# Optimization experiments

Measured on AMD Instinct MI355X. Metric: run time of the kernel, lower is better.

The kernel has to match this reference:

```python
import jax, jax.numpy as jnp
import numpy as np

B, SQ, SK, D = 8, 4096, 4096, 64


def setup_inputs() -> dict:
    key = jax.random.key(0)
    k1, k2, k3 = jax.random.split(key, 3)
    x1 = jax.random.normal(k1, (B, SQ, D), dtype=jnp.float32)   # queries
    x2 = jax.random.normal(k2, (B, SK, D), dtype=jnp.float32)   # keys
    x3 = jax.random.normal(k3, (B, SK, D), dtype=jnp.float32)   # values
    x4 = 0                                                      # dropout p (static, 0 => deterministic)
    x5 = jnp.ones((1,), dtype=jnp.float32)                      # scale divisor
    return {"x1": x1, "x2": x2, "x3": x3, "x4": x4, "x5": x5}


def reference(x1, x2, x3, x4, x5):
    # scores: [B, Sq, Sk]
    scores = jnp.einsum("bqd,bkd->bqk", x1, x2) / x5
    attn = jax.nn.softmax(scores, axis=-1)
    p = float(x4)  # static python scalar
    if p > 0.0:
        mask = jax.random.bernoulli(jax.random.key(42), 1.0 - p, attn.shape)
        attn = attn * mask.astype(attn.dtype) / (1.0 - p)
    # out: [B, Sq, D]
    return jnp.einsum("bqk,bkd->bqd", attn, x3)
```

## Files before the change

### kernel.cpp

```cpp
#include <hip/hip_runtime.h>


typedef _Float16 f16x8 __attribute__((ext_vector_type(8)));
typedef _Float16 f16x4 __attribute__((ext_vector_type(4)));
typedef __fp16   h16x2 __attribute__((ext_vector_type(2)));
typedef float    f32x4 __attribute__((ext_vector_type(4)));

constexpr int kB  = 8;
constexpr int kSQ = 4096;
constexpr int kSK = 4096;
constexpr int kD  = 64;
constexpr int KSPLIT = 4;
constexpr int SKH = kSK / KSPLIT;
constexpr int BQ  = 128;
constexpr int BK  = 64;
constexpr size_t APART = (size_t)kB * kSQ * kD;
constexpr float kLog2e = 1.44269504088896340736f;

static __device__ __forceinline__ f16x4 pack4(float a, float b, float c, float d) {
    h16x2 p0 = __builtin_amdgcn_cvt_pkrtz(a, b);
    h16x2 p1 = __builtin_amdgcn_cvt_pkrtz(c, d);
    f16x4 r;
    r[0] = (_Float16)p0[0]; r[1] = (_Float16)p0[1];
    r[2] = (_Float16)p1[0]; r[3] = (_Float16)p1[1];
    return r;
}
static __device__ __forceinline__ f16x8 pack8(const float4& a, const float4& c) {
    f16x4 lo = pack4(a.x, a.y, a.z, a.w);
    f16x4 hi = pack4(c.x, c.y, c.z, c.w);
    f16x8 f;
    f[0] = lo[0]; f[1] = lo[1]; f[2] = lo[2]; f[3] = lo[3];
    f[4] = hi[0]; f[5] = hi[1]; f[6] = hi[2]; f[7] = hi[3];
    return f;
}

typedef const __attribute__((address_space(1))) unsigned int* gu32p;
typedef __attribute__((address_space(3))) unsigned int* lu32p;
static __device__ __forceinline__ void gload_lds16(const void* g, void* l) {
    __builtin_amdgcn_global_load_lds((gu32p)g, (lu32p)l, 16, 0, 0);
}

__global__ __launch_bounds__(256, 2)
void fattn_prepass(const float* __restrict__ Kg,
                   const float* __restrict__ Vg,
                   _Float16* __restrict__ Kh,
                   _Float16* __restrict__ Vt)
{
    __shared__ _Float16 tr[kD][BK];

    const int tid = threadIdx.x;
    const int kt  = blockIdx.x;
    const int b   = blockIdx.y;

    const int k = tid >> 2;
    const int p = tid & 3;
    const int gk = kt * BK + k;

    {
        const float* src = Kg + ((size_t)b * kSK + gk) * kD + p * 16;
        const float4 a0 = *(const float4*)(src + 0);
        const float4 a1 = *(const float4*)(src + 4);
        const float4 a2 = *(const float4*)(src + 8);
        const float4 a3 = *(const float4*)(src + 12);
        _Float16* dst = Kh + ((size_t)b * kSK + gk) * kD;
        const int fb0 = 2 * p, fb1 = 2 * p + 1;
        *(f16x8*)&dst[(fb0 ^ (gk & 7)) * 8] = pack8(a0, a1);
        *(f16x8*)&dst[(fb1 ^ (gk & 7)) * 8] = pack8(a2, a3);
    }
    {
        const float* src = Vg + ((size_t)b * kSK + gk) * kD + p * 16;
        const float4 a0 = *(const float4*)(src + 0);
        const float4 a1 = *(const float4*)(src + 4);
        const float4 a2 = *(const float4*)(src + 8);
        const float4 a3 = *(const float4*)(src + 12);
        const float v[16] = {a0.x,a0.y,a0.z,a0.w, a1.x,a1.y,a1.z,a1.w,
                             a2.x,a2.y,a2.z,a2.w, a3.x,a3.y,a3.z,a3.w};
#pragma unroll
        for (int j = 0; j < 16; ++j)
            tr[p * 16 + j][k] = (_Float16)v[j];
    }
    __syncthreads();
    {
        const int f  = tid >> 2;
        const int p2 = tid & 3;
        const f16x8 b0 = *(const f16x8*)&tr[f][p2 * 16 + 0];
        const f16x8 b1 = *(const f16x8*)&tr[f][p2 * 16 + 8];
        _Float16* dst = Vt + (((size_t)b * 64 + kt) * kD + f) * BK;
        const int kb0 = 2 * p2, kb1 = 2 * p2 + 1;
        *(f16x8*)&dst[(kb0 ^ (f & 7)) * 8] = b0;
        *(f16x8*)&dst[(kb1 ^ (f & 7)) * 8] = b1;
    }
}

__global__ __launch_bounds__(256, 4)
void fattn_partial(const float* __restrict__ Qg,
                   const _Float16* __restrict__ Kh,
                   const _Float16* __restrict__ Vt,
                   const float* __restrict__ sdiv,
                   _Float16* __restrict__ Ap,
                   float2* __restrict__ MLp)
{
    __shared__ __align__(16) _Float16 sK[2][BK * kD];
    __shared__ __align__(16) _Float16 sV[2][kD * BK];
    __shared__ __align__(16) _Float16 sP[4][16][BK];

    const int tid  = threadIdx.x;
    const int w    = tid >> 6;
    const int lane = tid & 63;
    const int l16  = lane & 15;
    const int quad = lane >> 4;
    const int sw   = (quad ^ (l16 & 7)) * 8;
    const int swp  = (l16 & 7) * 8;

    const int flat = blockIdx.x;
    const int c    = flat & 31;
    const int qi   = flat >> 5;
    const int b    = c >> 2;
    const int ks   = c & 3;
    const int qb   = qi * BQ;

    const float qscale = kLog2e / sdiv[0];

    const float* Qb = Qg + ((size_t)b * kSQ + qb) * kD;
    const _Float16* Khb = Kh + ((size_t)b * kSK + (size_t)ks * SKH) * kD;
    const _Float16* Vtb = Vt + (((size_t)b * 64 + (size_t)ks * (SKH / BK)) * kD) * BK;

    f16x8 qf[2][2];
#pragma unroll
    for (int mt = 0; mt < 2; ++mt) {
        const float* qrow = Qb + (size_t)(w * 32 + mt * 16 + l16) * kD;
#pragma unroll
        for (int kk = 0; kk < 2; ++kk) {
            const float4 a = *(const float4*)(qrow + kk * 32 + quad * 8);
            const float4 cc = *(const float4*)(qrow + kk * 32 + quad * 8 + 4);
            float4 as = make_float4(a.x * qscale, a.y * qscale, a.z * qscale, a.w * qscale);
            float4 cs = make_float4(cc.x * qscale, cc.y * qscale, cc.z * qscale, cc.w * qscale);
            qf[mt][kk] = pack8(as, cs);
        }
    }

    auto stage = [&](int kt, int buf) {
        const char* gk = (const char*)(Khb + (size_t)kt * BK * kD) + w * 2048 + lane * 16;
        const char* gv = (const char*)(Vtb + (size_t)kt * kD * BK) + w * 2048 + lane * 16;
        char* lk = (char*)&sK[buf][0] + w * 2048;
        char* lv = (char*)&sV[buf][0] + w * 2048;
        gload_lds16(gk,        lk);
        gload_lds16(gk + 1024, lk + 1024);
        gload_lds16(gv,        lv);
        gload_lds16(gv + 1024, lv + 1024);
    };

    f32x4 o[2][4];
    float m_i[2] = {-1e30f, -1e30f}, l_i[2] = {0.0f, 0.0f};
#pragma unroll
    for (int mt = 0; mt < 2; ++mt)
#pragma unroll
        for (int dt = 0; dt < 4; ++dt)
#pragma unroll
            for (int r = 0; r < 4; ++r) o[mt][dt][r] = 0.0f;

    stage(0, 0);
    __syncthreads();

    const int nIter = SKH / BK;
    for (int kt = 0; kt < nIter; ++kt) {
        const int buf = kt & 1;
        const bool more = (kt + 1 < nIter);
        if (more) stage(kt + 1, buf ^ 1);

        f32x4 s[2][4];
#pragma unroll
        for (int nt = 0; nt < 4; ++nt) {
            const int krow = (nt * 16 + l16) * kD;
            const f16x8 kf0 = *(const f16x8*)&sK[buf][krow + sw];
            const f16x8 kf1 = *(const f16x8*)&sK[buf][krow + (sw ^ 32)];
#pragma unroll
            for (int mt = 0; mt < 2; ++mt) {
                f32x4 acc;
#pragma unroll
                for (int r = 0; r < 4; ++r) acc[r] = 0.0f;
                acc = __builtin_amdgcn_mfma_f32_16x16x32_f16(kf0, qf[mt][0], acc, 0, 0, 0);
                acc = __builtin_amdgcn_mfma_f32_16x16x32_f16(kf1, qf[mt][1], acc, 0, 0, 0);
                s[mt][nt] = acc;
            }
        }

        f16x8 vf[4][2];
#pragma unroll
        for (int dt = 0; dt < 4; ++dt) {
            const int frow = (dt * 16 + l16) * BK;
            vf[dt][0] = *(const f16x8*)&sV[buf][frow + sw];
            vf[dt][1] = *(const f16x8*)&sV[buf][frow + (sw ^ 32)];
        }

#pragma unroll
        for (int mt = 0; mt < 2; ++mt) {
            float ra = fmaxf(fmaxf(s[mt][0][0], s[mt][0][1]), fmaxf(s[mt][0][2], s[mt][0][3]));
            float rb = fmaxf(fmaxf(s[mt][1][0], s[mt][1][1]), fmaxf(s[mt][1][2], s[mt][1][3]));
            float rc = fmaxf(fmaxf(s[mt][2][0], s[mt][2][1]), fmaxf(s[mt][2][2], s[mt][2][3]));
            float rd = fmaxf(fmaxf(s[mt][3][0], s[mt][3][1]), fmaxf(s[mt][3][2], s[mt][3][3]));
            float rm = fmaxf(fmaxf(ra, rb), fmaxf(rc, rd));
            rm = fmaxf(rm, __shfl_xor(rm, 16, 64));
            rm = fmaxf(rm, __shfl_xor(rm, 32, 64));
            const float mnew = fmaxf(m_i[mt], rm);
            float rs = 0.0f;
#pragma unroll
            for (int nt = 0; nt < 4; ++nt)
#pragma unroll
                for (int r = 0; r < 4; ++r) {
                    const float p = __builtin_amdgcn_exp2f(s[mt][nt][r] - mnew);
                    s[mt][nt][r] = p;
                    rs += p;
                }
            rs += __shfl_xor(rs, 16, 64);
            rs += __shfl_xor(rs, 32, 64);
            if (!__all(mnew == m_i[mt])) {
                const float alpha = __builtin_amdgcn_exp2f(m_i[mt] - mnew);
                l_i[mt] *= alpha;
#pragma unroll
                for (int dt = 0; dt < 4; ++dt)
#pragma unroll
                    for (int r = 0; r < 4; ++r) o[mt][dt][r] *= alpha;
            }
            m_i[mt] = mnew;
            l_i[mt] += rs;

#pragma unroll
            for (int nt = 0; nt < 4; ++nt)
                *(f16x4*)&sP[w][l16][(nt * 16 + quad * 4) ^ swp] =
                    pack4(s[mt][nt][0], s[mt][nt][1], s[mt][nt][2], s[mt][nt][3]);

            const f16x8 pf0 = *(const f16x8*)&sP[w][l16][(quad * 8) ^ swp];
            const f16x8 pf1 = *(const f16x8*)&sP[w][l16][(32 + quad * 8) ^ swp];
#pragma unroll
            for (int dt = 0; dt < 4; ++dt) {
                o[mt][dt] = __builtin_amdgcn_mfma_f32_16x16x32_f16(vf[dt][0], pf0, o[mt][dt], 0, 0, 0);
                o[mt][dt] = __builtin_amdgcn_mfma_f32_16x16x32_f16(vf[dt][1], pf1, o[mt][dt], 0, 0, 0);
            }
        }

        __syncthreads();
    }

    _Float16* Ab = Ap + (size_t)ks * APART + ((size_t)b * kSQ + qb) * kD;
    float2* MLb = MLp + (size_t)ks * kB * kSQ + (size_t)b * kSQ + qb;
#pragma unroll
    for (int mt = 0; mt < 2; ++mt) {
        const int row = w * 32 + mt * 16 + l16;
#pragma unroll
        for (int dt = 0; dt < 4; ++dt)
            *(f16x4*)&Ab[(size_t)row * kD + dt * 16 + quad * 4] =
                pack4(o[mt][dt][0], o[mt][dt][1], o[mt][dt][2], o[mt][dt][3]);
        if (quad == 0) MLb[row] = make_float2(m_i[mt], l_i[mt]);
    }
}

__global__ __launch_bounds__(256)
void fattn_combine(const _Float16* __restrict__ Ap,
                   const float2* __restrict__ MLp,
                   float* __restrict__ Og)
{
    const int idx = blockIdx.x * 256 + threadIdx.x;
    const int r = idx >> 4;
    const int c = (idx & 15) * 4;

    float m = -1e30f;
    float2 ml[KSPLIT];
#pragma unroll
    for (int s = 0; s < KSPLIT; ++s) {
        ml[s] = MLp[(size_t)s * kB * kSQ + r];
        m = fmaxf(m, ml[s].x);
    }
    float acc[4] = {0.f, 0.f, 0.f, 0.f};
    float lsum = 0.f;
#pragma unroll
    for (int s = 0; s < KSPLIT; ++s) {
        const float e = __builtin_amdgcn_exp2f(ml[s].x - m);
        lsum += e * ml[s].y;
        const f16x4 a = *(const f16x4*)&Ap[(size_t)s * APART + (size_t)r * kD + c];
#pragma unroll
        for (int j = 0; j < 4; ++j) acc[j] += e * (float)a[j];
    }
    const float inv = 1.0f / lsum;
    float4 res = make_float4(acc[0] * inv, acc[1] * inv, acc[2] * inv, acc[3] * inv);
    *(float4*)&Og[(size_t)r * kD + c] = res;
}

extern "C" void kernel_launch(void* const* d_in, const int* in_sizes, int n_in,
                              void* d_out, int out_size, void* d_ws, size_t ws_size,
                              hipStream_t stream) {
    const float* Q    = (const float*)d_in[0];
    const float* K    = (const float*)d_in[1];
    const float* V    = (const float*)d_in[2];
    const float* sdiv = (const float*)d_in[4];
    float* O = (float*)d_out;

    _Float16* Kh  = (_Float16*)d_ws;
    _Float16* Vt  = Kh + (size_t)kB * kSK * kD;
    _Float16* Ap  = Vt + (size_t)kB * kSK * kD;
    float2*   MLp = (float2*)(Ap + (size_t)KSPLIT * APART);

    fattn_prepass<<<dim3(kSK / BK, kB), dim3(256), 0, stream>>>(K, V, Kh, Vt);
    fattn_partial<<<dim3((kSQ / BQ) * kB * KSPLIT), dim3(256), 0, stream>>>(Q, Kh, Vt, sdiv, Ap, MLp);
    fattn_combine<<<dim3(kB * kSQ * kD / (256 * 4)), dim3(256), 0, stream>>>(Ap, MLp, O);
}
```

Before: 145.8 us.

## Double query tile per block and compute row sums with MFMA against ones

Each block now handles 256 query rows, so each wave holds four 16-row tiles instead of two. This doubles reuse of every K/V tile staged into LDS and halves global K/V traffic per query. The softmax row-sum no longer uses scalar adds and cross-lane shuffles; it runs as extra MFMAs that multiply P by a vector of ones into a separate accumulator. In exchange, register pressure rises (launch bounds drop from 4 to 2 blocks per SM), occupancy falls, there are half as many blocks, and the row sum is accumulated from fp16-rounded P.

```diff
diff --git a/kernel.cpp b/kernel.cpp
--- a/kernel.cpp
+++ b/kernel.cpp
@@ -12,7 +12,8 @@
 constexpr int kD  = 64;
 constexpr int KSPLIT = 4;
 constexpr int SKH = kSK / KSPLIT;
-constexpr int BQ  = 128;
+constexpr int BQ  = 256;
+constexpr int MT  = 4;
 constexpr int BK  = 64;
 constexpr size_t APART = (size_t)kB * kSQ * kD;
 constexpr float kLog2e = 1.44269504088896340736f;
@@ -92,7 +93,7 @@
     }
 }
 
-__global__ __launch_bounds__(256, 4)
+__global__ __launch_bounds__(256, 2)
 void fattn_partial(const float* __restrict__ Qg,
                    const _Float16* __restrict__ Kh,
                    const _Float16* __restrict__ Vt,
@@ -125,10 +126,10 @@
     const _Float16* Khb = Kh + ((size_t)b * kSK + (size_t)ks * SKH) * kD;
     const _Float16* Vtb = Vt + (((size_t)b * 64 + (size_t)ks * (SKH / BK)) * kD) * BK;
 
-    f16x8 qf[2][2];
-#pragma unroll
-    for (int mt = 0; mt < 2; ++mt) {
-        const float* qrow = Qb + (size_t)(w * 32 + mt * 16 + l16) * kD;
+    f16x8 qf[MT][2];
+#pragma unroll
+    for (int mt = 0; mt < MT; ++mt) {
+        const float* qrow = Qb + (size_t)(w * 64 + mt * 16 + l16) * kD;
 #pragma unroll
         for (int kk = 0; kk < 2; ++kk) {
             const float4 a = *(const float4*)(qrow + kk * 32 + quad * 8);
@@ -138,6 +139,10 @@
             qf[mt][kk] = pack8(as, cs);
         }
     }
+
+    f16x8 ones;
+#pragma unroll
+    for (int j = 0; j < 8; ++j) ones[j] = (_Float16)1.0f;
 
     auto stage = [&](int kt, int buf) {
         const char* gk = (const char*)(Khb + (size_t)kt * BK * kD) + w * 2048 + lane * 16;
@@ -150,14 +155,19 @@
         gload_lds16(gv + 1024, lv + 1024);
     };
 
-    f32x4 o[2][4];
-    float m_i[2] = {-1e30f, -1e30f}, l_i[2] = {0.0f, 0.0f};
-#pragma unroll
-    for (int mt = 0; mt < 2; ++mt)
+    f32x4 o[MT][4];
+    f32x4 ol[MT];
+    float m_i[MT];
+#pragma unroll
+    for (int mt = 0; mt < MT; ++mt) {
+        m_i[mt] = -1e30f;
+#pragma unroll
+        for (int r = 0; r < 4; ++r) ol[mt][r] = 0.0f;
 #pragma unroll
         for (int dt = 0; dt < 4; ++dt)
 #pragma unroll
             for (int r = 0; r < 4; ++r) o[mt][dt][r] = 0.0f;
+    }
 
     stage(0, 0);
     __syncthreads();
@@ -168,14 +178,14 @@
         const bool more = (kt + 1 < nIter);
         if (more) stage(kt + 1, buf ^ 1);
 
-        f32x4 s[2][4];
+        f32x4 s[MT][4];
 #pragma unroll
         for (int nt = 0; nt < 4; ++nt) {
             const int krow = (nt * 16 + l16) * kD;
             const f16x8 kf0 = *(const f16x8*)&sK[buf][krow + sw];
             const f16x8 kf1 = *(const f16x8*)&sK[buf][krow + (sw ^ 32)];
 #pragma unroll
-            for (int mt = 0; mt < 2; ++mt) {
+            for (int mt = 0; mt < MT; ++mt) {
                 f32x4 acc;
 #pragma unroll
                 for (int r = 0; r < 4; ++r) acc[r] = 0.0f;
@@ -194,7 +204,7 @@
         }
 
 #pragma unroll
-        for (int mt = 0; mt < 2; ++mt) {
+        for (int mt = 0; mt < MT; ++mt) {
             float ra = fmaxf(fmaxf(s[mt][0][0], s[mt][0][1]), fmaxf(s[mt][0][2], s[mt][0][3]));
             float rb = fmaxf(fmaxf(s[mt][1][0], s[mt][1][1]), fmaxf(s[mt][1][2], s[mt][1][3]));
             float rc = fmaxf(fmaxf(s[mt][2][0], s[mt][2][1]), fmaxf(s[mt][2][2], s[mt][2][3]));
@@ -203,27 +213,20 @@
             rm = fmaxf(rm, __shfl_xor(rm, 16, 64));
             rm = fmaxf(rm, __shfl_xor(rm, 32, 64));
             const float mnew = fmaxf(m_i[mt], rm);
-            float rs = 0.0f;
 #pragma unroll
             for (int nt = 0; nt < 4; ++nt)
 #pragma unroll
-                for (int r = 0; r < 4; ++r) {
-                    const float p = __builtin_amdgcn_exp2f(s[mt][nt][r] - mnew);
-                    s[mt][nt][r] = p;
-                    rs += p;
-                }
-            rs += __shfl_xor(rs, 16, 64);
-            rs += __shfl_xor(rs, 32, 64);
+                for (int r = 0; r < 4; ++r)
+                    s[mt][nt][r] = __builtin_amdgcn_exp2f(s[mt][nt][r] - mnew);
             if (!__all(mnew == m_i[mt])) {
                 const float alpha = __builtin_amdgcn_exp2f(m_i[mt] - mnew);
-                l_i[mt] *= alpha;
+                ol[mt][0] *= alpha;
 #pragma unroll
                 for (int dt = 0; dt < 4; ++dt)
 #pragma unroll
                     for (int r = 0; r < 4; ++r) o[mt][dt][r] *= alpha;
             }
             m_i[mt] = mnew;
-            l_i[mt] += rs;
 
 #pragma unroll
             for (int nt = 0; nt < 4; ++nt)
@@ -237,6 +240,8 @@
                 o[mt][dt] = __builtin_amdgcn_mfma_f32_16x16x32_f16(vf[dt][0], pf0, o[mt][dt], 0, 0, 0);
                 o[mt][dt] = __builtin_amdgcn_mfma_f32_16x16x32_f16(vf[dt][1], pf1, o[mt][dt], 0, 0, 0);
             }
+            ol[mt] = __builtin_amdgcn_mfma_f32_16x16x32_f16(ones, pf0, ol[mt], 0, 0, 0);
+            ol[mt] = __builtin_amdgcn_mfma_f32_16x16x32_f16(ones, pf1, ol[mt], 0, 0, 0);
         }
 
         __syncthreads();
@@ -245,13 +250,13 @@
     _Float16* Ab = Ap + (size_t)ks * APART + ((size_t)b * kSQ + qb) * kD;
     float2* MLb = MLp + (size_t)ks * kB * kSQ + (size_t)b * kSQ + qb;
 #pragma unroll
-    for (int mt = 0; mt < 2; ++mt) {
-        const int row = w * 32 + mt * 16 + l16;
+    for (int mt = 0; mt < MT; ++mt) {
+        const int row = w * 64 + mt * 16 + l16;
 #pragma unroll
         for (int dt = 0; dt < 4; ++dt)
             *(f16x4*)&Ab[(size_t)row * kD + dt * 16 + quad * 4] =
                 pack4(o[mt][dt][0], o[mt][dt][1], o[mt][dt][2], o[mt][dt][3]);
-        if (quad == 0) MLb[row] = make_float2(m_i[mt], l_i[mt]);
+        if (quad == 0) MLb[row] = make_float2(m_i[mt], ol[mt][0]);
     }
 }
 
```

Result: faster. 138.0 us (-5.4%).
